# Kernel optimization log

Hardware: AMD Instinct MI355X
Metric: run time of the kernel (lower is better)

## Reference

```python
import jax, jax.numpy as jnp
import numpy as np

ALPHA = 0.25
GAMMA = 2.0
PROB_MIN = 0.0001


def _gather_feat(feat, inds):
    # feat: [B, C, H, W], inds: [B, K] in [0, H*W) -> [B, K, C]
    B, C, H, W = feat.shape
    f = feat.reshape(B, C, H * W).transpose(0, 2, 1)  # [B, HW, C]
    return jnp.take_along_axis(f, inds[:, :, None], axis=1)


def setup_inputs() -> dict:
    key = jax.random.key(0)
    ks = jax.random.split(key, 7)
    B, C, H, W, K = 8, 64, 152, 272, 500
    HW = H * W
    cur_reid = jax.random.normal(ks[0], (B, C, H, W), dtype=jnp.float32)
    pre_reid = jax.random.normal(ks[1], (B, C, H, W), dtype=jnp.float32)
    cur_inds = jax.random.randint(ks[2], (B, K), 0, HW, dtype=jnp.int64)
    pre_inds = jax.random.randint(ks[3], (B, K), 0, HW, dtype=jnp.int64)
    cur_circum_ind = jax.random.randint(ks[4], (B, K), 0, HW, dtype=jnp.int64)
    pre_circum_ind = jax.random.randint(ks[5], (B, K), 0, HW, dtype=jnp.int64)
    tracking_mask = jax.random.randint(ks[6], (B, K, 1), 0, 2, dtype=jnp.int32)
    return {
        "cur_reid": cur_reid,
        "pre_reid": pre_reid,
        "cur_inds": cur_inds,
        "pre_inds": pre_inds,
        "cur_circum_ind": cur_circum_ind,
        "pre_circum_ind": pre_circum_ind,
        "tracking_mask": tracking_mask,
    }


def reference(cur_reid, pre_reid, cur_inds, pre_inds, cur_circum_ind, pre_circum_ind, tracking_mask):
    mask = tracking_mask[:, :, 0].astype(jnp.int64)  # [B, K], 0/1
    # Replace indices of non-tracked slots with the pre-drawn random indices
    cur_idx = cur_inds * mask + cur_circum_ind * (1 - mask)
    pre_idx = pre_inds * mask + pre_circum_ind * (1 - mask)

    cur_feat = _gather_feat(cur_reid, cur_idx)  # [B, K, C]
    pre_feat = _gather_feat(pre_reid, pre_idx)  # [B, K, C]

    # similarity[b, i, j] = sigmoid(<cur_feat[b,i], pre_feat[b,j]>)
    sim = jax.nn.sigmoid(jnp.einsum("bic,bjc->bij", cur_feat, pre_feat))  # [B, K, K]

    # groundtruth = diag_embed(mask): gt[b,i,i] = mask[b,i]
    K = mask.shape[1]
    gt = mask[:, :, None] * jnp.eye(K, dtype=mask.dtype)[None]  # [B, K, K]

    # focal loss: p_t = sim if gt==1 else 1-sim; alpha_t = 0.25 if gt==1 else 0.75
    probs = jnp.where(gt == 1, sim, 1.0 - sim)
    probs = jnp.clip(probs, PROB_MIN, 1.0)
    alpha_t = jnp.where(gt == 1, ALPHA, 1.0 - ALPHA)
    loss = jnp.mean(-alpha_t * (1.0 - probs) ** GAMMA * jnp.log(probs))
    return loss
```

## Files before the change

kernel.cpp:

```cpp
#include <hip/hip_runtime.h>

#define B 8
#define C 64
#define H 152
#define W 272
#define HW (H * W)
#define K 500
#define ALPHA 0.25f
#define PROB_MIN 1e-4f

#define TS 32
#define NT ((K + TS - 1) / TS)
#define LDS_PAD 68

__global__ __launch_bounds__(128) void gather_kernel(
    const float* __restrict__ cur_reid,
    const float* __restrict__ pre_reid,
    const int* __restrict__ cur_inds,
    const int* __restrict__ pre_inds,
    const int* __restrict__ cur_circ,
    const int* __restrict__ pre_circ,
    const int* __restrict__ tmask,
    float* __restrict__ curf,
    float* __restrict__ pref,
    float* __restrict__ out)
{
    const int bk = blockIdx.x;
    const int t  = threadIdx.x;
    if (bk == 0 && t == 0) out[0] = 0.0f;

    const int b = bk / K;
    const int m = tmask[bk];
    if (t < C) {
        const int idx = m ? cur_inds[bk] : cur_circ[bk];
        curf[(size_t)bk * C + t] = cur_reid[((size_t)(b * C + t)) * HW + idx];
    } else {
        const int c = t - C;
        const int idx = m ? pre_inds[bk] : pre_circ[bk];
        pref[(size_t)bk * C + c] = pre_reid[((size_t)(b * C + c)) * HW + idx];
    }
}

__device__ __forceinline__ float focal_term(float x, int gi, int gj, int b,
                                            const int* __restrict__ tmask)
{
    if (gi >= K || gj >= K) return 0.0f;
    const float sim = 1.0f / (1.0f + __expf(-x));
    const int gt = (gi == gj) ? tmask[b * K + gi] : 0;
    float p = gt ? sim : 1.0f - sim;
    p = fminf(fmaxf(p, PROB_MIN), 1.0f);
    const float a = gt ? ALPHA : (1.0f - ALPHA);
    const float om = 1.0f - p;
    return a * om * om * (-__logf(p));
}

__global__ __launch_bounds__(256) void loss_kernel(
    const float* __restrict__ curf,
    const float* __restrict__ pref,
    const int* __restrict__ tmask,
    float* __restrict__ out)
{
    __shared__ float sc[TS][LDS_PAD];
    __shared__ float sp[TS][LDS_PAD];
    __shared__ float wsum[4];

    const int ti = blockIdx.x;
    const int tj = blockIdx.y;
    const int b  = blockIdx.z;
    const int t  = threadIdx.x;
    const int i0 = ti * TS;
    const int j0 = tj * TS;

#pragma unroll
    for (int r = 0; r < 2; ++r) {
        const int f   = t + r * 256;
        const int row = f >> 4;
        const int c4  = (f & 15) * 4;
        float4 va = make_float4(0.f, 0.f, 0.f, 0.f);
        float4 vb = make_float4(0.f, 0.f, 0.f, 0.f);
        const int gi = i0 + row;
        const int gj = j0 + row;
        if (gi < K) va = *(const float4*)&curf[((size_t)(b * K + gi)) * C + c4];
        if (gj < K) vb = *(const float4*)&pref[((size_t)(b * K + gj)) * C + c4];
        *(float4*)&sc[row][c4] = va;
        *(float4*)&sp[row][c4] = vb;
    }
    __syncthreads();

    const int tx = t & 15;
    const int ty = t >> 4;
    float a00 = 0.f, a01 = 0.f, a10 = 0.f, a11 = 0.f;

#pragma unroll
    for (int c = 0; c < C; c += 4) {
        const float4 x0 = *(const float4*)&sc[ty][c];
        const float4 x1 = *(const float4*)&sc[ty + 16][c];
        const float4 y0 = *(const float4*)&sp[tx][c];
        const float4 y1 = *(const float4*)&sp[tx + 16][c];
        a00 += x0.x * y0.x + x0.y * y0.y + x0.z * y0.z + x0.w * y0.w;
        a01 += x0.x * y1.x + x0.y * y1.y + x0.z * y1.z + x0.w * y1.w;
        a10 += x1.x * y0.x + x1.y * y0.y + x1.z * y0.z + x1.w * y0.w;
        a11 += x1.x * y1.x + x1.y * y1.y + x1.z * y1.z + x1.w * y1.w;
    }

    const int gi0 = i0 + ty, gi1 = i0 + ty + 16;
    const int gj0 = j0 + tx, gj1 = j0 + tx + 16;
    float s = focal_term(a00, gi0, gj0, b, tmask)
            + focal_term(a01, gi0, gj1, b, tmask)
            + focal_term(a10, gi1, gj0, b, tmask)
            + focal_term(a11, gi1, gj1, b, tmask);

#pragma unroll
    for (int o = 32; o > 0; o >>= 1) s += __shfl_down(s, o, 64);
    if ((t & 63) == 0) wsum[t >> 6] = s;
    __syncthreads();
    if (t == 0) {
        const float tot = wsum[0] + wsum[1] + wsum[2] + wsum[3];
        atomicAdd(out, tot * (1.0f / ((float)B * (float)K * (float)K)));
    }
}

extern "C" void kernel_launch(void* const* d_in, const int* in_sizes, int n_in,
                              void* d_out, int out_size, void* d_ws, size_t ws_size,
                              hipStream_t stream)
{
    const float* cur_reid = (const float*)d_in[0];
    const float* pre_reid = (const float*)d_in[1];
    const int*   cur_inds = (const int*)d_in[2];
    const int*   pre_inds = (const int*)d_in[3];
    const int*   cur_circ = (const int*)d_in[4];
    const int*   pre_circ = (const int*)d_in[5];
    const int*   tmask    = (const int*)d_in[6];
    float*       out      = (float*)d_out;

    float* curf = (float*)d_ws;
    float* pref = curf + (size_t)B * K * C;

    gather_kernel<<<B * K, 128, 0, stream>>>(
        cur_reid, pre_reid, cur_inds, pre_inds, cur_circ, pre_circ, tmask,
        curf, pref, out);

    dim3 grid(NT, NT, B);
    loss_kernel<<<grid, 256, 0, stream>>>(curf, pref, tmask, out);
}
```

Baseline: 198.6 us.

## Compute similarity with bf16 MFMA tiles over padded gathered features

```diff
diff --git a/kernel.cpp b/kernel.cpp
--- a/kernel.cpp
+++ b/kernel.cpp
@@ -6,12 +6,18 @@
 #define W 272
 #define HW (H * W)
 #define K 500
+#define KP 512
 #define ALPHA 0.25f
 #define PROB_MIN 1e-4f
 
-#define TS 32
-#define NT ((K + TS - 1) / TS)
-#define LDS_PAD 68
+typedef __attribute__((ext_vector_type(8))) short short8;
+typedef __attribute__((ext_vector_type(4))) float floatx4;
+
+__device__ __forceinline__ unsigned short f32_to_bf16(float f) {
+    union { float f; unsigned int u; } v; v.f = f;
+    unsigned int r = v.u + 0x7FFFu + ((v.u >> 16) & 1u);
+    return (unsigned short)(r >> 16);
+}
 
 __global__ __launch_bounds__(128) void gather_kernel(
     const float* __restrict__ cur_reid,
@@ -21,23 +27,34 @@
     const int* __restrict__ cur_circ,
     const int* __restrict__ pre_circ,
     const int* __restrict__ tmask,
-    float* __restrict__ curf,
-    float* __restrict__ pref,
+    unsigned short* __restrict__ curf,
+    unsigned short* __restrict__ pref,
     float* __restrict__ out)
 {
     const int bk = blockIdx.x;
     const int t  = threadIdx.x;
     if (bk == 0 && t == 0) out[0] = 0.0f;
 
-    const int b = bk / K;
-    const int m = tmask[bk];
+    const int b = bk >> 9;
+    const int k = bk & (KP - 1);
+
+    if (k >= K) {
+        if (t < C)      curf[(size_t)bk * C + t] = 0;
+        else            pref[(size_t)bk * C + (t - C)] = 0;
+        return;
+    }
+
+    const int bk_in = b * K + k;
+    const int m = tmask[bk_in];
     if (t < C) {
-        const int idx = m ? cur_inds[bk] : cur_circ[bk];
-        curf[(size_t)bk * C + t] = cur_reid[((size_t)(b * C + t)) * HW + idx];
+        const int idx = m ? cur_inds[bk_in] : cur_circ[bk_in];
+        const float v = cur_reid[((size_t)(b * C + t)) * HW + idx];
+        curf[(size_t)bk * C + t] = f32_to_bf16(v);
     } else {
         const int c = t - C;
-        const int idx = m ? pre_inds[bk] : pre_circ[bk];
-        pref[(size_t)bk * C + c] = pre_reid[((size_t)(b * C + c)) * HW + idx];
+        const int idx = m ? pre_inds[bk_in] : pre_circ[bk_in];
+        const float v = pre_reid[((size_t)(b * C + c)) * HW + idx];
+        pref[(size_t)bk * C + c] = f32_to_bf16(v);
     }
 }
 
@@ -54,68 +71,56 @@
     return a * om * om * (-__logf(p));
 }
 
-__global__ __launch_bounds__(256) void loss_kernel(
-    const float* __restrict__ curf,
-    const float* __restrict__ pref,
+#define LOSS_THREADS 1024
+
+__global__ __launch_bounds__(LOSS_THREADS) void loss_kernel(
+    const unsigned short* __restrict__ curf,
+    const unsigned short* __restrict__ pref,
     const int* __restrict__ tmask,
     float* __restrict__ out)
 {
-    __shared__ float sc[TS][LDS_PAD];
-    __shared__ float sp[TS][LDS_PAD];
-    __shared__ float wsum[4];
+    __shared__ float wsum[LOSS_THREADS / 64];
 
-    const int ti = blockIdx.x;
-    const int tj = blockIdx.y;
-    const int b  = blockIdx.z;
-    const int t  = threadIdx.x;
-    const int i0 = ti * TS;
-    const int j0 = tj * TS;
+    const int t    = threadIdx.x;
+    const int wave = t >> 6;
+    const int lane = t & 63;
 
+    const int tile = blockIdx.x * (LOSS_THREADS / 64) + wave;
+    const int b    = tile >> 10;
+    const int rem  = tile & 1023;
+    const int ti   = rem >> 5;
+    const int tj   = rem & 31;
+
+    const int m16  = lane & 15;
+    const int quad = lane >> 4;
+
+    const unsigned short* pa = curf + (((size_t)(b * KP + ti * 16 + m16)) * C + quad * 8);
+    const unsigned short* pb = pref + (((size_t)(b * KP + tj * 16 + m16)) * C + quad * 8);
+    const short8 a0 = *(const short8*)pa;
+    const short8 a1 = *(const short8*)(pa + 32);
+    const short8 b0 = *(const short8*)pb;
+    const short8 b1 = *(const short8*)(pb + 32);
+
+    floatx4 acc = {0.f, 0.f, 0.f, 0.f};
+    acc = __builtin_amdgcn_mfma_f32_16x16x32_bf16(a0, b0, acc, 0, 0, 0);
+    acc = __builtin_amdgcn_mfma_f32_16x16x32_bf16(a1, b1, acc, 0, 0, 0);
+
+    const int gj = tj * 16 + m16;
+    float s = 0.f;
 #pragma unroll
-    for (int r = 0; r < 2; ++r) {
-        const int f   = t + r * 256;
-        const int row = f >> 4;
-        const int c4  = (f & 15) * 4;
-        float4 va = make_float4(0.f, 0.f, 0.f, 0.f);
-        float4 vb = make_float4(0.f, 0.f, 0.f, 0.f);
-        const int gi = i0 + row;
-        const int gj = j0 + row;
-        if (gi < K) va = *(const float4*)&curf[((size_t)(b * K + gi)) * C + c4];
-        if (gj < K) vb = *(const float4*)&pref[((size_t)(b * K + gj)) * C + c4];
-        *(float4*)&sc[row][c4] = va;
-        *(float4*)&sp[row][c4] = vb;
+    for (int r = 0; r < 4; ++r) {
+        const int gi = ti * 16 + quad * 4 + r;
+        s += focal_term(acc[r], gi, gj, b, tmask);
     }
-    __syncthreads();
-
-    const int tx = t & 15;
-    const int ty = t >> 4;
-    float a00 = 0.f, a01 = 0.f, a10 = 0.f, a11 = 0.f;
-
-#pragma unroll
-    for (int c = 0; c < C; c += 4) {
-        const float4 x0 = *(const float4*)&sc[ty][c];
-        const float4 x1 = *(const float4*)&sc[ty + 16][c];
-        const float4 y0 = *(const float4*)&sp[tx][c];
-        const float4 y1 = *(const float4*)&sp[tx + 16][c];
-        a00 += x0.x * y0.x + x0.y * y0.y + x0.z * y0.z + x0.w * y0.w;
-        a01 += x0.x * y1.x + x0.y * y1.y + x0.z * y1.z + x0.w * y1.w;
-        a10 += x1.x * y0.x + x1.y * y0.y + x1.z * y0.z + x1.w * y0.w;
-        a11 += x1.x * y1.x + x1.y * y1.y + x1.z * y1.z + x1.w * y1.w;
-    }
-
-    const int gi0 = i0 + ty, gi1 = i0 + ty + 16;
-    const int gj0 = j0 + tx, gj1 = j0 + tx + 16;
-    float s = focal_term(a00, gi0, gj0, b, tmask)
-            + focal_term(a01, gi0, gj1, b, tmask)
-            + focal_term(a10, gi1, gj0, b, tmask)
-            + focal_term(a11, gi1, gj1, b, tmask);
 
 #pragma unroll
     for (int o = 32; o > 0; o >>= 1) s += __shfl_down(s, o, 64);
-    if ((t & 63) == 0) wsum[t >> 6] = s;
+    if (lane == 0) wsum[wave] = s;
     __syncthreads();
     if (t == 0) {
-        const float tot = wsum[0] + wsum[1] + wsum[2] + wsum[3];
+        float tot = 0.f;
+#pragma unroll
+        for (int w = 0; w < LOSS_THREADS / 64; ++w) tot += wsum[w];
         atomicAdd(out, tot * (1.0f / ((float)B * (float)K * (float)K)));
     }
 }
@@ -133,13 +138,12 @@
     const int*   tmask    = (const int*)d_in[6];
     float*       out      = (float*)d_out;
 
-    float* curf = (float*)d_ws;
-    float* pref = curf + (size_t)B * K * C;
+    unsigned short* curf = (unsigned short*)d_ws;
+    unsigned short* pref = curf + (size_t)B * KP * C;
 
-    gather_kernel<<<B * K, 128, 0, stream>>>(
+    gather_kernel<<<B * KP, 128, 0, stream>>>(
         cur_reid, pre_reid, cur_inds, pre_inds, cur_circ, pre_circ, tmask,
         curf, pref, out);
 
-    dim3 grid(NT, NT, B);
-    loss_kernel<<<grid, 256, 0, stream>>>(curf, pref, tmask, out);
+    loss_kernel<<<512, LOSS_THREADS, 0, stream>>>(curf, pref, tmask, out);
 }
```

Result: faster. 176.4 us (-11.2%).
